# Kernel tuning notes

Hardware: AMD Instinct MI355X
Metric: run time of the kernel (lower is better)

Reference implementation:

```python
import jax, jax.numpy as jnp
import numpy as np

B, R, S = 4, 32768, 64
NEAR, FAR = -1.5, 1.5
DELTA_INF = 1e10
EPS = 1e-10


def setup_inputs() -> dict:
    key = jax.random.key(0)
    k1, k2 = jax.random.split(key)
    rgb = jax.random.uniform(k1, (B, R, S, 3), dtype=jnp.float32)
    sigma = jax.random.normal(k2, (B, R, S, 1), dtype=jnp.float32)
    # stratified-like depths: monotonically increasing along sample axis per ray
    z_steps = jnp.linspace(0.0, 1.0, S, dtype=jnp.float32)  # [S]
    z_vals = (NEAR * (1.0 - z_steps) + FAR * z_steps)[None, None, :, None]
    z_vals = jnp.broadcast_to(z_vals, (B, R, S, 1)).astype(jnp.float32)
    return {"rgb": rgb, "sigma": sigma, "z_vals": z_vals}


def reference(rgb, sigma, z_vals):
    """fancy_integration with clamp_mode='relu', noise_std=0, white_back=False, last_back=False.

    rgb:    [B, R, S, 3]
    sigma:  [B, R, S, 1]
    z_vals: [B, R, S, 1] (sorted along S)
    Returns (rgb_final [B,R,3], depth_final [B,R,1], weights [B,R,S,1]).
    """
    # deltas between consecutive samples; last delta is 'infinite'
    deltas = z_vals[:, :, 1:] - z_vals[:, :, :-1]                      # [B,R,S-1,1]
    delta_inf = jnp.full_like(deltas[:, :, :1], DELTA_INF)
    deltas = jnp.concatenate([deltas, delta_inf], axis=2)              # [B,R,S,1]

    # sigma -> alpha: 1 - exp(-relu(sigma) * delta)
    alphas = 1.0 - jnp.exp(-deltas * jax.nn.relu(sigma))               # [B,R,S,1]

    # exclusive cumprod transmittance along sample axis
    alphas_shifted = jnp.concatenate(
        [jnp.ones_like(alphas[:, :, :1]), 1.0 - alphas + EPS], axis=2)  # [B,R,S+1,1]
    transmittance = jnp.cumprod(alphas_shifted, axis=2)[:, :, :-1]      # [B,R,S,1]
    weights = alphas * transmittance                                    # [B,R,S,1]

    rgb_final = jnp.sum(weights * rgb, axis=2)      # [B,R,3]
    depth_final = jnp.sum(weights * z_vals, axis=2)  # [B,R,1]
    return (rgb_final, depth_final, weights)
```

## Files before the change

kernel.cpp:

```cpp
#include <hip/hip_runtime.h>


#define EPS_W 1e-10f
#define DELTA_INF_V 1e10f

#define DPP_ROW_SHL(n) (0x100 | (n))
#define DPP_ROW_SHR(n) (0x110 | (n))

using f4 = __attribute__((ext_vector_type(4))) float;

template <int CTRL>
__device__ __forceinline__ float dpp_mov(float x, float old) {
    return __builtin_bit_cast(float,
        __builtin_amdgcn_update_dpp(
            __builtin_bit_cast(int, old), __builtin_bit_cast(int, x),
            CTRL, 0xf, 0xf, false));
}

__device__ __forceinline__ float row_scan_mul(float p) {
    p *= dpp_mov<DPP_ROW_SHR(1)>(p, 1.0f);
    p *= dpp_mov<DPP_ROW_SHR(2)>(p, 1.0f);
    p *= dpp_mov<DPP_ROW_SHR(4)>(p, 1.0f);
    p *= dpp_mov<DPP_ROW_SHR(8)>(p, 1.0f);
    return p;
}

__device__ __forceinline__ float row_sum(float x) {
    x += dpp_mov<DPP_ROW_SHR(1)>(x, 0.0f);
    x += dpp_mov<DPP_ROW_SHR(2)>(x, 0.0f);
    x += dpp_mov<DPP_ROW_SHR(4)>(x, 0.0f);
    x += dpp_mov<DPP_ROW_SHR(8)>(x, 0.0f);
    return x;
}

__global__ __launch_bounds__(256) void volrend_kernel(
    const float* __restrict__ rgb,
    const float* __restrict__ sigma,
    const float* __restrict__ z_vals,
    float* __restrict__ rgb_out,
    float* __restrict__ depth_out,
    float* __restrict__ weights_out,
    int n_rays)
{
    const int lane = threadIdx.x & 63;
    const int wave = threadIdx.x >> 6;
    const long long wave_g = (long long)blockIdx.x * (blockDim.x >> 6) + wave;

    const int j   = lane & 15;
    const int row = lane >> 4;
    const long long ray = wave_g * 4 + row;
    if (ray >= n_rays) return;

    const f4 sg = __builtin_nontemporal_load(
        reinterpret_cast<const f4*>(sigma + wave_g * 256) + lane);
    const f4 zz = __builtin_nontemporal_load(
        reinterpret_cast<const f4*>(z_vals + wave_g * 256) + lane);
    const f4* rgb4 = reinterpret_cast<const f4*>(rgb + wave_g * 768 + (long long)lane * 12);
    const f4 c0 = __builtin_nontemporal_load(rgb4 + 0);
    const f4 c1 = __builtin_nontemporal_load(rgb4 + 1);
    const f4 c2 = __builtin_nontemporal_load(rgb4 + 2);

    const float zn = dpp_mov<DPP_ROW_SHL(1)>(zz.x, 0.0f);
    const float d0 = zz.y - zz.x;
    const float d1 = zz.z - zz.y;
    const float d2 = zz.w - zz.z;
    const float d3 = (j == 15) ? DELTA_INF_V : (zn - zz.w);

    const float a0 = 1.0f - __expf(-d0 * fmaxf(sg.x, 0.0f));
    const float a1 = 1.0f - __expf(-d1 * fmaxf(sg.y, 0.0f));
    const float a2 = 1.0f - __expf(-d2 * fmaxf(sg.z, 0.0f));
    const float a3 = 1.0f - __expf(-d3 * fmaxf(sg.w, 0.0f));

    const float q0 = 1.0f - a0 + EPS_W;
    const float q1 = 1.0f - a1 + EPS_W;
    const float q2 = 1.0f - a2 + EPS_W;
    const float q3 = 1.0f - a3 + EPS_W;
    const float P0 = q0;
    const float P1 = P0 * q1;
    const float P2 = P1 * q2;
    const float P3 = P2 * q3;

    const float R = row_scan_mul(P3);
    const float E = dpp_mov<DPP_ROW_SHR(1)>(R, 1.0f);

    const float T0 = E;
    const float T1 = E * P0;
    const float T2 = E * P1;
    const float T3 = E * P2;

    const float w0 = a0 * T0;
    const float w1 = a1 * T1;
    const float w2 = a2 * T2;
    const float w3 = a3 * T3;

    f4 wv; wv.x = w0; wv.y = w1; wv.z = w2; wv.w = w3;
    __builtin_nontemporal_store(
        wv, reinterpret_cast<f4*>(weights_out + wave_g * 256) + lane);

    float pr = w0 * c0.x + w1 * c0.w + w2 * c1.z + w3 * c2.y;
    float pg = w0 * c0.y + w1 * c1.x + w2 * c1.w + w3 * c2.z;
    float pb = w0 * c0.z + w1 * c1.y + w2 * c2.x + w3 * c2.w;
    float pd = w0 * zz.x + w1 * zz.y + w2 * zz.z + w3 * zz.w;

    pr = row_sum(pr);
    pg = row_sum(pg);
    pb = row_sum(pb);
    pd = row_sum(pd);

    if (j == 15) {
        __builtin_nontemporal_store(pr, rgb_out + ray * 3 + 0);
        __builtin_nontemporal_store(pg, rgb_out + ray * 3 + 1);
        __builtin_nontemporal_store(pb, rgb_out + ray * 3 + 2);
        __builtin_nontemporal_store(pd, depth_out + ray);
    }
}

extern "C" void kernel_launch(void* const* d_in, const int* in_sizes, int n_in,
                              void* d_out, int out_size, void* d_ws, size_t ws_size,
                              hipStream_t stream) {
    const float* rgb    = (const float*)d_in[0];
    const float* sigma  = (const float*)d_in[1];
    const float* z_vals = (const float*)d_in[2];

    const int n_rays = in_sizes[1] / 64;

    float* out         = (float*)d_out;
    float* rgb_out     = out;
    float* depth_out   = out + (long long)n_rays * 3;
    float* weights_out = out + (long long)n_rays * 4;

    const int block = 256;
    const int rays_per_block = (block / 64) * 4;
    const int grid = (n_rays + rays_per_block - 1) / rays_per_block;

    volrend_kernel<<<grid, block, 0, stream>>>(
        rgb, sigma, z_vals, rgb_out, depth_out, weights_out, n_rays);
}
```

Before: 193.4 us.

## Process multiple ray chunks per wave with double-buffered prefetch

Each wave now walks up to eight 4-ray chunks with a grid stride, prefetching the next chunk's sigma, z and rgb into a second register buffer while the current chunk is computed. The grid shrinks by the same factor. The goal is to overlap memory latency with computation and cut per-block launch overhead in this bandwidth-bound kernel. In exchange it uses more registers, and with fewer waves in flight the hardware has less parallelism for hiding latency. Ray counts not divisible by 4 are now dropped by the chunk count.

```diff
diff --git a/kernel.cpp b/kernel.cpp
--- a/kernel.cpp
+++ b/kernel.cpp
@@ -6,6 +6,8 @@
 
 #define DPP_ROW_SHL(n) (0x100 | (n))
 #define DPP_ROW_SHR(n) (0x110 | (n))
+
+#define TPW 8
 
 using f4 = __attribute__((ext_vector_type(4))) float;
 
@@ -45,73 +47,90 @@
     const int lane = threadIdx.x & 63;
     const int wave = threadIdx.x >> 6;
     const long long wave_g = (long long)blockIdx.x * (blockDim.x >> 6) + wave;
+    const long long W = (long long)gridDim.x * (blockDim.x >> 6);
 
     const int j   = lane & 15;
     const int row = lane >> 4;
-    const long long ray = wave_g * 4 + row;
-    if (ray >= n_rays) return;
+    const long long n_chunks = n_rays >> 2;
 
-    const f4 sg = __builtin_nontemporal_load(
-        reinterpret_cast<const f4*>(sigma + wave_g * 256) + lane);
-    const f4 zz = __builtin_nontemporal_load(
-        reinterpret_cast<const f4*>(z_vals + wave_g * 256) + lane);
-    const f4* rgb4 = reinterpret_cast<const f4*>(rgb + wave_g * 768 + (long long)lane * 12);
-    const f4 c0 = __builtin_nontemporal_load(rgb4 + 0);
-    const f4 c1 = __builtin_nontemporal_load(rgb4 + 1);
-    const f4 c2 = __builtin_nontemporal_load(rgb4 + 2);
+    f4 sgb[2], zzb[2], c0b[2], c1b[2], c2b[2];
 
-    const float zn = dpp_mov<DPP_ROW_SHL(1)>(zz.x, 0.0f);
-    const float d0 = zz.y - zz.x;
-    const float d1 = zz.z - zz.y;
-    const float d2 = zz.w - zz.z;
-    const float d3 = (j == 15) ? DELTA_INF_V : (zn - zz.w);
+    auto load_chunk = [&](long long ch, int b) {
+        sgb[b] = __builtin_nontemporal_load(
+            reinterpret_cast<const f4*>(sigma + ch * 256) + lane);
+        zzb[b] = __builtin_nontemporal_load(
+            reinterpret_cast<const f4*>(z_vals + ch * 256) + lane);
+        const f4* rgb4 = reinterpret_cast<const f4*>(rgb + ch * 768 + (long long)lane * 12);
+        c0b[b] = __builtin_nontemporal_load(rgb4 + 0);
+        c1b[b] = __builtin_nontemporal_load(rgb4 + 1);
+        c2b[b] = __builtin_nontemporal_load(rgb4 + 2);
+    };
 
-    const float a0 = 1.0f - __expf(-d0 * fmaxf(sg.x, 0.0f));
-    const float a1 = 1.0f - __expf(-d1 * fmaxf(sg.y, 0.0f));
-    const float a2 = 1.0f - __expf(-d2 * fmaxf(sg.z, 0.0f));
-    const float a3 = 1.0f - __expf(-d3 * fmaxf(sg.w, 0.0f));
+    auto process_chunk = [&](long long ch, int b) {
+        const f4 sg = sgb[b], zz = zzb[b];
+        const f4 c0 = c0b[b], c1 = c1b[b], c2 = c2b[b];
 
-    const float q0 = 1.0f - a0 + EPS_W;
-    const float q1 = 1.0f - a1 + EPS_W;
-    const float q2 = 1.0f - a2 + EPS_W;
-    const float q3 = 1.0f - a3 + EPS_W;
-    const float P0 = q0;
-    const float P1 = P0 * q1;
-    const float P2 = P1 * q2;
-    const float P3 = P2 * q3;
+        const float zn = dpp_mov<DPP_ROW_SHL(1)>(zz.x, 0.0f);
+        const float d0 = zz.y - zz.x;
+        const float d1 = zz.z - zz.y;
+        const float d2 = zz.w - zz.z;
+        const float d3 = (j == 15) ? DELTA_INF_V : (zn - zz.w);
 
-    const float R = row_scan_mul(P3);
-    const float E = dpp_mov<DPP_ROW_SHR(1)>(R, 1.0f);
+        const float a0 = 1.0f - __expf(-d0 * fmaxf(sg.x, 0.0f));
+        const float a1 = 1.0f - __expf(-d1 * fmaxf(sg.y, 0.0f));
+        const float a2 = 1.0f - __expf(-d2 * fmaxf(sg.z, 0.0f));
+        const float a3 = 1.0f - __expf(-d3 * fmaxf(sg.w, 0.0f));
 
-    const float T0 = E;
-    const float T1 = E * P0;
-    const float T2 = E * P1;
-    const float T3 = E * P2;
+        const float q0 = 1.0f - a0 + EPS_W;
+        const float q1 = 1.0f - a1 + EPS_W;
+        const float q2 = 1.0f - a2 + EPS_W;
+        const float q3 = 1.0f - a3 + EPS_W;
+        const float P0 = q0;
+        const float P1 = P0 * q1;
+        const float P2 = P1 * q2;
+        const float P3 = P2 * q3;
 
-    const float w0 = a0 * T0;
-    const float w1 = a1 * T1;
-    const float w2 = a2 * T2;
-    const float w3 = a3 * T3;
+        const float R = row_scan_mul(P3);
+        const float E = dpp_mov<DPP_ROW_SHR(1)>(R, 1.0f);
 
-    f4 wv; wv.x = w0; wv.y = w1; wv.z = w2; wv.w = w3;
-    __builtin_nontemporal_store(
-        wv, reinterpret_cast<f4*>(weights_out + wave_g * 256) + lane);
+        const float w0 = a0 * E;
+        const float w1 = a1 * (E * P0);
+        const float w2 = a2 * (E * P1);
+        const float w3 = a3 * (E * P2);
 
-    float pr = w0 * c0.x + w1 * c0.w + w2 * c1.z + w3 * c2.y;
-    float pg = w0 * c0.y + w1 * c1.x + w2 * c1.w + w3 * c2.z;
-    float pb = w0 * c0.z + w1 * c1.y + w2 * c2.x + w3 * c2.w;
-    float pd = w0 * zz.x + w1 * zz.y + w2 * zz.z + w3 * zz.w;
+        f4 wv; wv.x = w0; wv.y = w1; wv.z = w2; wv.w = w3;
+        __builtin_nontemporal_store(
+            wv, reinterpret_cast<f4*>(weights_out + ch * 256) + lane);
 
-    pr = row_sum(pr);
-    pg = row_sum(pg);
-    pb = row_sum(pb);
-    pd = row_sum(pd);
+        float pr = w0 * c0.x + w1 * c0.w + w2 * c1.z + w3 * c2.y;
+        float pg = w0 * c0.y + w1 * c1.x + w2 * c1.w + w3 * c2.z;
+        float pb = w0 * c0.z + w1 * c1.y + w2 * c2.x + w3 * c2.w;
+        float pd = w0 * zz.x + w1 * zz.y + w2 * zz.z + w3 * zz.w;
 
-    if (j == 15) {
-        __builtin_nontemporal_store(pr, rgb_out + ray * 3 + 0);
-        __builtin_nontemporal_store(pg, rgb_out + ray * 3 + 1);
-        __builtin_nontemporal_store(pb, rgb_out + ray * 3 + 2);
-        __builtin_nontemporal_store(pd, depth_out + ray);
+        pr = row_sum(pr);
+        pg = row_sum(pg);
+        pb = row_sum(pb);
+        pd = row_sum(pd);
+
+        if (j == 15) {
+            const long long ray = ch * 4 + row;
+            __builtin_nontemporal_store(pr, rgb_out + ray * 3 + 0);
+            __builtin_nontemporal_store(pg, rgb_out + ray * 3 + 1);
+            __builtin_nontemporal_store(pb, rgb_out + ray * 3 + 2);
+            __builtin_nontemporal_store(pd, depth_out + ray);
+        }
+    };
+
+    if (wave_g >= n_chunks) return;
+    load_chunk(wave_g, 0);
+
+    #pragma unroll
+    for (int t = 0; t < TPW; ++t) {
+        const long long cur = wave_g + (long long)t * W;
+        if (cur >= n_chunks) break;
+        const long long nxt = cur + W;
+        if ((t + 1 < TPW) && (nxt < n_chunks)) load_chunk(nxt, (t + 1) & 1);
+        process_chunk(cur, t & 1);
     }
 }
 
@@ -130,8 +149,9 @@
     float* weights_out = out + (long long)n_rays * 4;
 
     const int block = 256;
-    const int rays_per_block = (block / 64) * 4;
-    const int grid = (n_rays + rays_per_block - 1) / rays_per_block;
+    const int n_chunks = n_rays / 4;
+    const int chunks_per_block = (block / 64) * TPW;
+    const int grid = (n_chunks + chunks_per_block - 1) / chunks_per_block;
 
     volrend_kernel<<<grid, block, 0, stream>>>(
         rgb, sigma, z_vals, rgb_out, depth_out, weights_out, n_rays);
```

After: 197.6 us. 1.02x slower.
